# Kernel tuning notes

Measured on AMD Instinct MI355X. Metric: run time of the kernel, lower is better.

The kernel has to match this reference:

```python
import jax, jax.numpy as jnp
import numpy as np

HIDDEN = 4096
NH = 32        # num attention heads
NKV = 8        # num key/value heads
HD = 128       # q/k head dim
VHD = 96       # v head dim
ROT = 64       # rotary dim = int(HD * 0.5)
THETA = 10000.0
B, S = 2, 2048


def setup_inputs() -> dict:
    key = jax.random.key(0)
    ks = jax.random.split(key, 6)
    w = 0.02
    return {
        "hidden_states": jax.random.normal(ks[0], (B, S, HIDDEN), jnp.float32),
        "position_ids": jnp.arange(B * S, dtype=jnp.int32).reshape(B, S) % S,
        "Wq": jax.random.normal(ks[1], (NH * HD, HIDDEN), jnp.float32) * w,
        "Wk": jax.random.normal(ks[2], (NKV * HD, HIDDEN), jnp.float32) * w,
        "Wv": jax.random.normal(ks[3], (NKV * VHD, HIDDEN), jnp.float32) * w,
        "Wo": jax.random.normal(ks[4], (HIDDEN, NH * VHD), jnp.float32) * w,
    }


def _rotate_half(x):
    x1, x2 = x[..., : x.shape[-1] // 2], x[..., x.shape[-1] // 2 :]
    return jnp.concatenate((-x2, x1), axis=-1)


def reference(hidden_states, position_ids, Wq, Wk, Wv, Wo):
    b, s, _ = hidden_states.shape
    # QKV projections (torch Linear: y = x @ W^T)
    q = (hidden_states @ Wq.T).reshape(b, s, NH, HD).transpose(0, 2, 1, 3)   # [b,NH,s,HD]
    k = (hidden_states @ Wk.T).reshape(b, s, NKV, HD).transpose(0, 2, 1, 3)  # [b,NKV,s,HD]
    v = (hidden_states @ Wv.T).reshape(b, s, NKV, VHD).transpose(0, 2, 1, 3)  # [b,NKV,s,VHD]

    # rotary embedding over first ROT dims (partial RoPE)
    inv_freq = 1.0 / (THETA ** (jnp.arange(0, ROT, 2, dtype=jnp.float32) / ROT))  # [ROT/2]
    freqs = position_ids.astype(jnp.float32)[:, :, None] * inv_freq              # [b,s,ROT/2]
    emb = jnp.concatenate((freqs, freqs), axis=-1)                                # [b,s,ROT]
    cos = jnp.cos(emb)[:, None, :, :].astype(hidden_states.dtype)                 # [b,1,s,ROT]
    sin = jnp.sin(emb)[:, None, :, :].astype(hidden_states.dtype)

    q_rot, q_pass = q[..., :ROT], q[..., ROT:]
    k_rot, k_pass = k[..., :ROT], k[..., ROT:]
    q_rot = q_rot * cos + _rotate_half(q_rot) * sin
    k_rot = k_rot * cos + _rotate_half(k_rot) * sin
    q = jnp.concatenate((q_rot, q_pass), axis=-1)
    k = jnp.concatenate((k_rot, k_pass), axis=-1)

    # GQA: repeat_kv (repeat_interleave over head dim)
    n_rep = NH // NKV
    k = jnp.repeat(k, n_rep, axis=1)  # [b,NH,s,HD]
    v = jnp.repeat(v, n_rep, axis=1)  # [b,NH,s,VHD]

    scores = jnp.einsum("bhqd,bhkd->bhqk", q, k) / np.float32(np.sqrt(HD))
    # causal additive mask (attention_mask as built by the HF model)
    neg = jnp.finfo(jnp.float32).min
    causal = jnp.where(jnp.tril(jnp.ones((s, s), dtype=bool)), 0.0, neg)
    scores = scores + causal[None, None, :, :]

    attn = jax.nn.softmax(scores.astype(jnp.float32), axis=-1).astype(q.dtype)
    out = jnp.einsum("bhqk,bhkd->bhqd", attn, v)          # [b,NH,s,VHD]
    out = out.transpose(0, 2, 1, 3).reshape(b, s, NH * VHD)
    return out @ Wo.T                                      # [b,s,HIDDEN]
```

## Files before the change

### kernel.cpp

```cpp
#include <hip/hip_runtime.h>

typedef __attribute__((ext_vector_type(4))) float f32x4;
typedef __attribute__((ext_vector_type(8))) __bf16 bf16x8;
typedef __attribute__((ext_vector_type(8))) unsigned short u16x8;
typedef __attribute__((ext_vector_type(4))) unsigned short u16x4;
typedef __attribute__((ext_vector_type(4))) short s16x4;
typedef unsigned short ushort_t;

__device__ __forceinline__ unsigned short f2bf(float x) {
  unsigned u = __builtin_bit_cast(unsigned, x);
  u += 0x7fffu + ((u >> 16) & 1u);
  return (unsigned short)(u >> 16);
}
__device__ __forceinline__ float bf2f(unsigned short h) {
  unsigned u = ((unsigned)h) << 16;
  return __builtin_bit_cast(float, u);
}
__device__ __forceinline__ short f2bf_n(float x) {
  return __builtin_bit_cast(short, (__bf16)x);
}

__device__ __forceinline__ void gload_lds16(const void* g, void* l) {
  __builtin_amdgcn_global_load_lds(
      (const __attribute__((address_space(1))) unsigned int*)g,
      (__attribute__((address_space(3))) unsigned int*)l, 16, 0, 0);
}

__global__ __launch_bounds__(256) void k_xw_to_bf16(
    const float* __restrict__ X, const float* __restrict__ Wq,
    const float* __restrict__ Wk, const float* __restrict__ Wv,
    const float* __restrict__ Wo,
    ushort_t* __restrict__ dX, ushort_t* __restrict__ dWq,
    ushort_t* __restrict__ dWk, ushort_t* __restrict__ dWv,
    ushort_t* __restrict__ dWo) {
  const int b = blockIdx.x;
  const float* src;
  ushort_t* dst;
  int i;
  if (b < 8192)       { src = X;  dst = dX;  i = b * 256 + threadIdx.x; }
  else if (b < 16384) { src = Wq; dst = dWq; i = (b - 8192) * 256 + threadIdx.x; }
  else if (b < 18432) { src = Wk; dst = dWk; i = (b - 16384) * 256 + threadIdx.x; }
  else if (b < 19968) { src = Wv; dst = dWv; i = (b - 18432) * 256 + threadIdx.x; }
  else                { src = Wo; dst = dWo; i = (b - 19968) * 256 + threadIdx.x; }
  float4 a = ((const float4*)src)[i * 2 + 0];
  float4 c = ((const float4*)src)[i * 2 + 1];
  u16x8 o;
  o[0] = f2bf(a.x); o[1] = f2bf(a.y); o[2] = f2bf(a.z); o[3] = f2bf(a.w);
  o[4] = f2bf(c.x); o[5] = f2bf(c.y); o[6] = f2bf(c.z); o[7] = f2bf(c.w);
  ((u16x8*)dst)[i] = o;
}

template <int OUT_BF16, int ROPE>
__global__ __launch_bounds__(256, 4) void k_gemm_bt(
    const ushort_t* __restrict__ A, const ushort_t* __restrict__ B,
    void* __restrict__ C, int K, int lda, int ldb, int ldc,
    const int* __restrict__ pos_ids) {
  __shared__ ushort_t lA[128 * 64];
  __shared__ ushort_t lB[128 * 64];
  const int t = threadIdx.x;
  const int ln = t & 63, w = t >> 6;
  const int fr = ln & 15, fg = ln >> 4;
  const int m0 = blockIdx.x * 128, n0 = blockIdx.y * 128;
  const int wr = (w >> 1) * 64, wc = (w & 1) * 64;

  const int srow = t >> 3;
  const int scol = ((((t & 7) * 16) ^ ((srow & 7) << 4)) >> 1);
  const ushort_t* pA = A + (srow + m0) * lda + scol;
  const ushort_t* pB = B + (srow + n0) * ldb + scol;
  char* lAb = (char*)lA + (w << 10);
  char* lBb = (char*)lB + (w << 10);

  f32x4 acc[4][4] = {};

  for (int k0 = 0; k0 < K; k0 += 64) {
    __syncthreads();
#pragma unroll
    for (int i = 0; i < 4; ++i) {
      gload_lds16(pA + i * 32 * lda + k0, lAb + i * 4096);
      gload_lds16(pB + i * 32 * ldb + k0, lBb + i * 4096);
    }
    __syncthreads();
#pragma unroll
    for (int kh = 0; kh < 2; ++kh) {
      bf16x8 af[4], bfv[4];
#pragma unroll
      for (int m = 0; m < 4; ++m) {
        int row = wr + m * 16 + fr;
        af[m] = *(const bf16x8*)((const char*)lA + row * 128 +
                                 ((kh * 64 + fg * 16) ^ ((row & 7) << 4)));
      }
#pragma unroll
      for (int n = 0; n < 4; ++n) {
        int row = wc + n * 16 + fr;
        bfv[n] = *(const bf16x8*)((const char*)lB + row * 128 +
                                  ((kh * 64 + fg * 16) ^ ((row & 7) << 4)));
      }
#pragma unroll
      for (int m = 0; m < 4; ++m)
#pragma unroll
        for (int n = 0; n < 4; ++n)
          acc[m][n] = __builtin_amdgcn_mfma_f32_16x16x32_bf16(
              af[m], bfv[n], acc[m][n], 0, 0, 0);
    }
  }

  if (ROPE) {
    if (n0 < 5120 && wc == 0) {
#pragma unroll
      for (int n = 0; n < 2; ++n) {
        const float fi = (float)(n * 16 + fr);
        const float inv = exp2f(-fi * (13.287712379549449f / 32.0f));
#pragma unroll
        for (int m = 0; m < 4; ++m) {
          const int row = m0 + wr + m * 16 + fg * 4;
#pragma unroll
          for (int j = 0; j < 4; ++j) {
            const float ang = (float)pos_ids[row + j] * inv;
            float sn, cs;
            __sincosf(ang, &sn, &cs);
            const float x1 = acc[m][n][j], x2 = acc[m][n + 2][j];
            acc[m][n][j]     = x1 * cs - x2 * sn;
            acc[m][n + 2][j] = x2 * cs + x1 * sn;
          }
        }
      }
    }
  }

#pragma unroll
  for (int m = 0; m < 4; ++m)
#pragma unroll
    for (int n = 0; n < 4; ++n) {
      int row = m0 + wr + m * 16 + fg * 4;
      int col = n0 + wc + n * 16 + fr;
#pragma unroll
      for (int j = 0; j < 4; ++j) {
        if (OUT_BF16)
          ((ushort_t*)C)[(size_t)(row + j) * ldc + col] = f2bf(acc[m][n][j]);
        else
          ((float*)C)[(size_t)(row + j) * ldc + col] = acc[m][n][j];
      }
    }
}

__global__ __launch_bounds__(512, 2) void k_attn(
    const ushort_t* __restrict__ QKV, ushort_t* __restrict__ O) {
  __shared__ ushort_t lK[128 * 128];
  __shared__ ushort_t lV[32 * 100 * 4];

  const int t = threadIdx.x, ln = t & 63, w = t >> 6;
  const int fr = ln & 15, fg = ln >> 4;
  const int h = blockIdx.y, b = blockIdx.z;
  const int qt = b ? (7 - (int)blockIdx.x) : (int)blockIdx.x;
  const int hk = h >> 2;
  const int q0 = qt * 256 + w * 32;
  const int tb = b * 2048;

  bf16x8 qf[2][4];
#pragma unroll
  for (int rq = 0; rq < 2; ++rq)
#pragma unroll
    for (int kb = 0; kb < 4; ++kb)
      qf[rq][kb] = *(const bf16x8*)(QKV +
                    (size_t)(tb + q0 + rq * 16 + fr) * 5888 + h * 128 +
                    kb * 32 + fg * 8);

  f32x4 oacc[6][2] = {};
  float lreg[2] = {0.f, 0.f};

  const int krow = t >> 4;
  const int kse = ((((t & 15) * 16) ^ (((t >> 4) & 7) << 4)) >> 1);
  const int k4s = t / 12, c8s = t % 12;

  const float sc = 0.088388347648318447f;
  const float l2e = 1.4426950408889634f;
  const float scl2e = sc * l2e;
  const float MB = 16.0f * l2e;

  u16x8 vrow[4];
  const ushort_t* pVb =
      QKV + (size_t)(tb + k4s * 4) * 5888 + 5120 + hk * 96 + c8s * 8;
  if (t < 384) {
#pragma unroll
    for (int kr = 0; kr < 4; ++kr)
      vrow[kr] = *(const u16x8*)(pVb + (size_t)kr * 5888);
  }

  const int nkt = (qt + 1) * 2;
  for (int kt = 0; kt < nkt; ++kt) {
    const int kb0t = kt * 128;
    __syncthreads();
    if (t < 384) {
#pragma unroll
      for (int i = 0; i < 8; ++i) {
        int cs = (c8s * 8 + i) ^ (k4s & 15);
        u16x4 q;
#pragma unroll
        for (int kr = 0; kr < 4; ++kr) q[kr] = vrow[kr][i];
        *(u16x4*)(&lV[(k4s * 100 + cs) * 4]) = q;
      }
    }
    {
      const ushort_t* pK =
          QKV + (size_t)(tb + kb0t + krow) * 5888 + 4096 + hk * 128 + kse;
#pragma unroll
      for (int i = 0; i < 4; ++i)
        gload_lds16(pK + (size_t)i * 32 * 5888,
                    (char*)lK + i * 8192 + (w << 10));
    }
    __builtin_amdgcn_sched_barrier(0);
    const bool pre = (kt + 1 < nkt);
    if (pre && t < 384) {
      const ushort_t* pV = pVb + (size_t)(kb0t + 128) * 5888;
#pragma unroll
      for (int kr = 0; kr < 4; ++kr)
        vrow[kr] = *(const u16x8*)(pV + (size_t)kr * 5888);
    }
    __builtin_amdgcn_sched_barrier(0);
    if (pre && w < 6)
      asm volatile("s_waitcnt vmcnt(4) lgkmcnt(0)" ::: "memory");
    else
      asm volatile("s_waitcnt vmcnt(0) lgkmcnt(0)" ::: "memory");
    __builtin_amdgcn_s_barrier();
    asm volatile("" ::: "memory");
    __builtin_amdgcn_sched_barrier(0);

#pragma unroll
    for (int h64 = 0; h64 < 2; ++h64) {
      const int kb0 = kb0t + h64 * 64;
      if (kb0 > q0 + 31) break;
      f32x4 s[4][2] = {};
      __builtin_amdgcn_s_setprio(1);
#pragma unroll
      for (int cb = 0; cb < 4; ++cb) {
        const int kv = h64 * 64 + cb * 16 + fr;
        bf16x8 kf[4];
#pragma unroll
        for (int kb = 0; kb < 4; ++kb)
          kf[kb] = *(const bf16x8*)((const char*)lK + kv * 256 +
                                    ((kb * 64 + fg * 16) ^ ((kv & 7) << 4)));
#pragma unroll
        for (int rq = 0; rq < 2; ++rq)
#pragma unroll
          for (int kb = 0; kb < 4; ++kb)
            s[cb][rq] = __builtin_amdgcn_mfma_f32_16x16x32_bf16(
                kf[kb], qf[rq][kb], s[cb][rq], 0, 0, 0);
      }
      __builtin_amdgcn_s_setprio(0);
      if (kb0 + 63 > q0) {
#pragma unroll
        for (int rq = 0; rq < 2; ++rq) {
          const int qrel = q0 + rq * 16 + fr - kb0;
#pragma unroll
          for (int cb = 0; cb < 4; ++cb)
#pragma unroll
            for (int j = 0; j < 4; ++j)
              if (cb * 16 + fg * 4 + j > qrel) s[cb][rq][j] = -3.0e38f;
        }
      }
      s16x4 pb[4][2];
#pragma unroll
      for (int rq = 0; rq < 2; ++rq) {
        f32x4 ps4 = {};
#pragma unroll
        for (int cb = 0; cb < 4; ++cb) {
#pragma unroll
          for (int j = 0; j < 4; ++j) {
            float p = exp2f(fmaf(s[cb][rq][j], scl2e, -MB));
            s[cb][rq][j] = p;
            ps4[j] += p;
          }
        }
        lreg[rq] += (ps4[0] + ps4[1]) + (ps4[2] + ps4[3]);
#pragma unroll
        for (int cb = 0; cb < 4; ++cb) {
          s16x4 v;
#pragma unroll
          for (int j = 0; j < 4; ++j) v[j] = f2bf_n(s[cb][rq][j]);
          pb[cb][rq] = v;
        }
      }
      __builtin_amdgcn_s_setprio(1);
#pragma unroll
      for (int cb = 0; cb < 4; ++cb) {
        const int k4 = h64 * 16 + cb * 4 + fg;
        s16x4 va[6];
#pragma unroll
        for (int c6 = 0; c6 < 6; ++c6)
          va[c6] = *(const s16x4*)(
              &lV[((k4 * 100 + (((c6 * 16 + fr) ^ (k4 & 15))))) * 4]);
#pragma unroll
        for (int c6 = 0; c6 < 6; ++c6)
#pragma unroll
          for (int rq = 0; rq < 2; ++rq)
            oacc[c6][rq] = __builtin_amdgcn_mfma_f32_16x16x16bf16_1k(
                va[c6], pb[cb][rq], oacc[c6][rq], 0, 0, 0);
      }
      __builtin_amdgcn_s_setprio(0);
    }
  }
#pragma unroll
  for (int rq = 0; rq < 2; ++rq) {
    float l = lreg[rq];
    l += __shfl_xor(l, 16, 64);
    l += __shfl_xor(l, 32, 64);
    const float inv = 1.0f / l;
    const size_t rowb = (size_t)(tb + q0 + rq * 16 + fr) * 3072 + h * 96;
#pragma unroll
    for (int c6 = 0; c6 < 6; ++c6) {
      u16x4 o;
#pragma unroll
      for (int j = 0; j < 4; ++j)
        o[j] = (unsigned short)f2bf_n(oacc[c6][rq][j] * inv);
      *(u16x4*)(&O[rowb + c6 * 16 + fg * 4]) = o;
    }
  }
}

extern "C" void kernel_launch(void* const* d_in, const int* in_sizes, int n_in,
                              void* d_out, int out_size, void* d_ws,
                              size_t ws_size, hipStream_t stream) {
  const float* X  = (const float*)d_in[0];
  const int*   pos = (const int*)d_in[1];
  const float* Wq = (const float*)d_in[2];
  const float* Wk = (const float*)d_in[3];
  const float* Wv = (const float*)d_in[4];
  const float* Wo = (const float*)d_in[5];
  float* out = (float*)d_out;

  ushort_t* Xb    = (ushort_t*)d_ws;
  ushort_t* Wob   = Xb + 16777216;
  ushort_t* QKV   = Wob + 12582912;
  ushort_t* AO    = QKV + 24117248;
  ushort_t* Wqkvb = (ushort_t*)d_out;

  k_xw_to_bf16<<<26112, 256, 0, stream>>>(X, Wq, Wk, Wv, Wo, Xb, Wqkvb,
                                          Wqkvb + 16777216,
                                          Wqkvb + 20971520, Wob);

  k_gemm_bt<1, 1><<<dim3(32, 46), 256, 0, stream>>>(Xb, Wqkvb, QKV, 4096,
                                                    4096, 4096, 5888, pos);
  k_attn<<<dim3(8, 32, 2), 512, 0, stream>>>(QKV, AO);
  k_gemm_bt<0, 0><<<dim3(32, 32), 256, 0, stream>>>(AO, Wob, out, 3072, 3072,
                                                    3072, 4096, nullptr);
}
```

Before: 438.7 us.

## Double-buffer K/V LDS tiles in attention with 64-row key steps

The attention kernel now uses two 64-row K and V shared-memory buffers instead of one 128-row buffer. Loads for the next tile are issued before computing the current one, and one barrier sits at the end of each step, so global-to-LDS traffic can overlap with MFMA work. This costs more loop iterations and more barriers per key range. The prologue also issues a redundant V load with an odd offset that is immediately overwritten.

```diff
diff --git a/kernel.cpp b/kernel.cpp
--- a/kernel.cpp
+++ b/kernel.cpp
@@ -145,8 +145,8 @@
 
 __global__ __launch_bounds__(512, 2) void k_attn(
     const ushort_t* __restrict__ QKV, ushort_t* __restrict__ O) {
-  __shared__ ushort_t lK[128 * 128];
-  __shared__ ushort_t lV[32 * 100 * 4];
+  __shared__ ushort_t lK[2][64 * 128];
+  __shared__ ushort_t lV[2][16 * 97 * 4];
 
   const int t = threadIdx.x, ln = t & 63, w = t >> 6;
   const int fr = ln & 15, fg = ln >> 4;
@@ -177,67 +177,91 @@
   const float scl2e = sc * l2e;
   const float MB = 16.0f * l2e;
 
-  u16x8 vrow[4];
   const ushort_t* pVb =
       QKV + (size_t)(tb + k4s * 4) * 5888 + 5120 + hk * 96 + c8s * 8;
-  if (t < 384) {
+  const ushort_t* pKb =
+      QKV + (size_t)(tb + krow) * 5888 + 4096 + hk * 128 + kse;
+
+  const int nkt = qt * 4 + 4;
+  u16x8 vrow[4];
+
+  if (t < 192) {
 #pragma unroll
     for (int kr = 0; kr < 4; ++kr)
       vrow[kr] = *(const u16x8*)(pVb + (size_t)kr * 5888);
   }
-
-  const int nkt = (qt + 1) * 2;
+#pragma unroll
+  for (int i = 0; i < 2; ++i)
+    gload_lds16(pKb + (size_t)i * 32 * 5888,
+                (char*)&lK[0][0] + i * 8192 + (w << 10));
+  __builtin_amdgcn_sched_barrier(0);
+  if (t < 192) {
+#pragma unroll
+    for (int i = 0; i < 8; ++i) {
+      int cs = (c8s * 8 + i) ^ (k4s & 15);
+      u16x4 q;
+#pragma unroll
+      for (int kr = 0; kr < 4; ++kr) q[kr] = vrow[kr][i];
+      *(u16x4*)(&lV[0][(k4s * 97 + cs) * 4]) = q;
+    }
+#pragma unroll
+    for (int kr = 0; kr < 4; ++kr)
+      vrow[kr] = *(const u16x8*)(pVb + (size_t)(64 + kr * 4) * 5888 / 4 * 4);
+  }
+  if (t < 192) {
+    const ushort_t* pV1 = pVb + (size_t)64 * 5888;
+#pragma unroll
+    for (int kr = 0; kr < 4; ++kr)
+      vrow[kr] = *(const u16x8*)(pV1 + (size_t)kr * 5888);
+  }
+  __builtin_amdgcn_sched_barrier(0);
+  if (w < 3)
+    asm volatile("s_waitcnt vmcnt(4) lgkmcnt(0)" ::: "memory");
+  else
+    asm volatile("s_waitcnt vmcnt(0) lgkmcnt(0)" ::: "memory");
+  __builtin_amdgcn_s_barrier();
+  asm volatile("" ::: "memory");
+  __builtin_amdgcn_sched_barrier(0);
+
   for (int kt = 0; kt < nkt; ++kt) {
-    const int kb0t = kt * 128;
-    __syncthreads();
-    if (t < 384) {
+    const int kb0 = kt * 64;
+    const int cur = kt & 1, nxt = cur ^ 1;
+    const bool pre1 = (kt + 1 < nkt), pre2 = (kt + 2 < nkt);
+    if (pre1) {
+      const ushort_t* pK = pKb + (size_t)(kb0 + 64) * 5888;
+#pragma unroll
+      for (int i = 0; i < 2; ++i)
+        gload_lds16(pK + (size_t)i * 32 * 5888,
+                    (char*)&lK[nxt][0] + i * 8192 + (w << 10));
+    }
+    __builtin_amdgcn_sched_barrier(0);
+    if (pre1 && t < 192) {
 #pragma unroll
       for (int i = 0; i < 8; ++i) {
         int cs = (c8s * 8 + i) ^ (k4s & 15);
         u16x4 q;
 #pragma unroll
         for (int kr = 0; kr < 4; ++kr) q[kr] = vrow[kr][i];
-        *(u16x4*)(&lV[(k4s * 100 + cs) * 4]) = q;
-      }
-    }
-    {
-      const ushort_t* pK =
-          QKV + (size_t)(tb + kb0t + krow) * 5888 + 4096 + hk * 128 + kse;
-#pragma unroll
-      for (int i = 0; i < 4; ++i)
-        gload_lds16(pK + (size_t)i * 32 * 5888,
-                    (char*)lK + i * 8192 + (w << 10));
+        *(u16x4*)(&lV[nxt][(k4s * 97 + cs) * 4]) = q;
+      }
+      if (pre2) {
+        const ushort_t* pV = pVb + (size_t)(kb0 + 128) * 5888;
+#pragma unroll
+        for (int kr = 0; kr < 4; ++kr)
+          vrow[kr] = *(const u16x8*)(pV + (size_t)kr * 5888);
+      }
     }
     __builtin_amdgcn_sched_barrier(0);
-    const bool pre = (kt + 1 < nkt);
-    if (pre && t < 384) {
-      const ushort_t* pV = pVb + (size_t)(kb0t + 128) * 5888;
-#pragma unroll
-      for (int kr = 0; kr < 4; ++kr)
-        vrow[kr] = *(const u16x8*)(pV + (size_t)kr * 5888);
-    }
-    __builtin_amdgcn_sched_barrier(0);
-    if (pre && w < 6)
-      asm volatile("s_waitcnt vmcnt(4) lgkmcnt(0)" ::: "memory");
-    else
-      asm volatile("s_waitcnt vmcnt(0) lgkmcnt(0)" ::: "memory");
-    __builtin_amdgcn_s_barrier();
-    asm volatile("" ::: "memory");
-    __builtin_amdgcn_sched_barrier(0);
-
-#pragma unroll
-    for (int h64 = 0; h64 < 2; ++h64) {
-      const int kb0 = kb0t + h64 * 64;
-      if (kb0 > q0 + 31) break;
+    if (kb0 <= q0 + 31) {
       f32x4 s[4][2] = {};
       __builtin_amdgcn_s_setprio(1);
 #pragma unroll
       for (int cb = 0; cb < 4; ++cb) {
-        const int kv = h64 * 64 + cb * 16 + fr;
+        const int kv = cb * 16 + fr;
         bf16x8 kf[4];
 #pragma unroll
         for (int kb = 0; kb < 4; ++kb)
-          kf[kb] = *(const bf16x8*)((const char*)lK + kv * 256 +
+          kf[kb] = *(const bf16x8*)((const char*)&lK[cur][0] + kv * 256 +
                                     ((kb * 64 + fg * 16) ^ ((kv & 7) << 4)));
 #pragma unroll
         for (int rq = 0; rq < 2; ++rq)
@@ -283,12 +307,12 @@
       __builtin_amdgcn_s_setprio(1);
 #pragma unroll
       for (int cb = 0; cb < 4; ++cb) {
-        const int k4 = h64 * 16 + cb * 4 + fg;
+        const int k4 = cb * 4 + fg;
         s16x4 va[6];
 #pragma unroll
         for (int c6 = 0; c6 < 6; ++c6)
           va[c6] = *(const s16x4*)(
-              &lV[((k4 * 100 + (((c6 * 16 + fr) ^ (k4 & 15))))) * 4]);
+              &lV[cur][(k4 * 97 + (((c6 * 16 + fr) ^ (k4 & 15)))) * 4]);
 #pragma unroll
         for (int c6 = 0; c6 < 6; ++c6)
 #pragma unroll
@@ -297,6 +321,16 @@
                 va[c6], pb[cb][rq], oacc[c6][rq], 0, 0, 0);
       }
       __builtin_amdgcn_s_setprio(0);
+    }
+    if (pre1) {
+      __builtin_amdgcn_sched_barrier(0);
+      if (pre2 && w < 3)
+        asm volatile("s_waitcnt vmcnt(4) lgkmcnt(0)" ::: "memory");
+      else
+        asm volatile("s_waitcnt vmcnt(0) lgkmcnt(0)" ::: "memory");
+      __builtin_amdgcn_s_barrier();
+      asm volatile("" ::: "memory");
+      __builtin_amdgcn_sched_barrier(0);
     }
   }
 #pragma unroll
```

New measurement: 461.2 us. 5.1% more time.
